# Optimization experiments

Hardware: AMD Instinct MI355X
Metric: run time of the kernel (lower is better)

Reference implementation:

```python
import jax, jax.numpy as jnp
import numpy as np

I_DIM, H_DIM, SEQ, OUT = 2048, 2048, 4096, 2048

def setup_inputs() -> dict:
    key = jax.random.key(0)
    ks = jax.random.split(key, 8)
    s_i = 1.0 / np.sqrt(H_DIM)
    return {
        "input_seq": jax.random.normal(ks[0], (1, SEQ, I_DIM), dtype=jnp.float32),
        "W_ih": jax.random.uniform(ks[1], (4 * H_DIM, I_DIM), minval=-s_i, maxval=s_i, dtype=jnp.float32),
        "W_hh": jax.random.uniform(ks[2], (4 * H_DIM, H_DIM), minval=-s_i, maxval=s_i, dtype=jnp.float32),
        "b_ih": jax.random.uniform(ks[3], (4 * H_DIM,), minval=-s_i, maxval=s_i, dtype=jnp.float32),
        "b_hh": jax.random.uniform(ks[4], (4 * H_DIM,), minval=-s_i, maxval=s_i, dtype=jnp.float32),
        "W_fc": jax.random.uniform(ks[5], (OUT, H_DIM), minval=-s_i, maxval=s_i, dtype=jnp.float32),
        "b_fc": jax.random.uniform(ks[6], (OUT,), minval=-s_i, maxval=s_i, dtype=jnp.float32),
    }

def _lstm_last_h(x, W_ih, W_hh, b_ih, b_hh):
    # x: [B, S, I]. PyTorch gate order: i, f, g, o along the 4H axis.
    B, S, _ = x.shape
    H = W_hh.shape[1]
    # Precompute input contribution for all timesteps: [B, S, 4H]
    xg = jnp.einsum('bsi,gi->bsg', x, W_ih) + b_ih + b_hh

    def step(carry, xg_t):
        h, c = carry  # [B, H] each
        g = xg_t + h @ W_hh.T  # [B, 4H]
        i_g = jax.nn.sigmoid(g[:, 0 * H:1 * H])
        f_g = jax.nn.sigmoid(g[:, 1 * H:2 * H])
        g_g = jnp.tanh(g[:, 2 * H:3 * H])
        o_g = jax.nn.sigmoid(g[:, 3 * H:4 * H])
        c = f_g * c + i_g * g_g
        h = o_g * jnp.tanh(c)
        return (h, c), None

    h0 = jnp.zeros((B, H), dtype=x.dtype)
    c0 = jnp.zeros((B, H), dtype=x.dtype)
    (h_last, _), _ = jax.lax.scan(step, (h0, c0), jnp.swapaxes(xg, 0, 1))
    return h_last  # [B, H]

def reference(input_seq, W_ih, W_hh, b_ih, b_hh, W_fc, b_fc):
    h_last = _lstm_last_h(input_seq, W_ih, W_hh, b_ih, b_hh)
    # Original does predictions.view(1, -1) then fc; valid only for batch=1.
    pred = h_last.reshape(1, -1) @ W_fc.T + b_fc  # [1, OUT]
    return pred
```

## Files before the change

### kernel.cpp

```cpp
#include <hip/hip_runtime.h>
#include <hip/hip_bf16.h>
#include <hip/hip_fp16.h>

#define SEQ   4096
#define IDIM  2048
#define HDIM  2048
#define G4    8192
#define NBLK  256
#define NREP  8

typedef __attribute__((ext_vector_type(8))) short short8;
typedef __attribute__((ext_vector_type(4))) float f32x4;

__device__ __forceinline__ float fast_sig(float x) {
    float e = __builtin_amdgcn_exp2f(-1.4426950408889634f * x);
    return __builtin_amdgcn_rcpf(1.0f + e);
}
__device__ __forceinline__ float fast_tanh(float x) {
    float e = __builtin_amdgcn_exp2f(2.8853900817779268f * x);
    return 1.0f - 2.0f * __builtin_amdgcn_rcpf(e + 1.0f);
}
__device__ __forceinline__ unsigned short f2h(float f) {
    __half h = __float2half_rn(f);
    union { __half h; unsigned short s; } c; c.h = h; return c.s;
}
__device__ __forceinline__ float h2f(unsigned short u) {
    union { unsigned short s; __half h; } c; c.s = u; return __half2float(c.h);
}

#define GM 128
#define GN 128
#define GK 32
#define APAD 40

__global__ __launch_bounds__(256, 2)
void xg_gemm(const float* __restrict__ x, const float* __restrict__ Wih,
             const float* __restrict__ bih, const float* __restrict__ bhh,
             __hip_bfloat16* __restrict__ xg)
{
    __shared__ __hip_bfloat16 As[GM][APAD];
    __shared__ __hip_bfloat16 Bs[GN][APAD];

    const int t  = threadIdx.x;
    const int g0 = blockIdx.x * GN;
    const int s0 = blockIdx.y * GM;
    const int w  = t >> 6, L = t & 63;
    const int quad = L >> 4, lane16 = L & 15;
    const int wm = w >> 1, wn = w & 1;

    f32x4 acc[4][4];
#pragma unroll
    for (int mt = 0; mt < 4; ++mt)
#pragma unroll
        for (int nt = 0; nt < 4; ++nt) acc[mt][nt] = (f32x4){0.f, 0.f, 0.f, 0.f};

    const int srow = t >> 1, shalf = t & 1;
    const float* xp = x   + (size_t)(s0 + srow) * IDIM + 16 * shalf;
    const float* wp = Wih + (size_t)(g0 + srow) * IDIM + 16 * shalf;

    for (int k0 = 0; k0 < IDIM; k0 += GK) {
        float4 a0 = *(const float4*)(xp + k0);
        float4 a1 = *(const float4*)(xp + k0 + 4);
        float4 a2 = *(const float4*)(xp + k0 + 8);
        float4 a3 = *(const float4*)(xp + k0 + 12);
        float4 b0 = *(const float4*)(wp + k0);
        float4 b1 = *(const float4*)(wp + k0 + 4);
        float4 b2 = *(const float4*)(wp + k0 + 8);
        float4 b3 = *(const float4*)(wp + k0 + 12);
        __syncthreads();
        {
            union { __hip_bfloat16 h[8]; uint4 u; } pk;
            pk.h[0]=__float2bfloat16(a0.x); pk.h[1]=__float2bfloat16(a0.y);
            pk.h[2]=__float2bfloat16(a0.z); pk.h[3]=__float2bfloat16(a0.w);
            pk.h[4]=__float2bfloat16(a1.x); pk.h[5]=__float2bfloat16(a1.y);
            pk.h[6]=__float2bfloat16(a1.z); pk.h[7]=__float2bfloat16(a1.w);
            *(uint4*)&As[srow][16 * shalf] = pk.u;
            pk.h[0]=__float2bfloat16(a2.x); pk.h[1]=__float2bfloat16(a2.y);
            pk.h[2]=__float2bfloat16(a2.z); pk.h[3]=__float2bfloat16(a2.w);
            pk.h[4]=__float2bfloat16(a3.x); pk.h[5]=__float2bfloat16(a3.y);
            pk.h[6]=__float2bfloat16(a3.z); pk.h[7]=__float2bfloat16(a3.w);
            *(uint4*)&As[srow][16 * shalf + 8] = pk.u;
            pk.h[0]=__float2bfloat16(b0.x); pk.h[1]=__float2bfloat16(b0.y);
            pk.h[2]=__float2bfloat16(b0.z); pk.h[3]=__float2bfloat16(b0.w);
            pk.h[4]=__float2bfloat16(b1.x); pk.h[5]=__float2bfloat16(b1.y);
            pk.h[6]=__float2bfloat16(b1.z); pk.h[7]=__float2bfloat16(b1.w);
            *(uint4*)&Bs[srow][16 * shalf] = pk.u;
            pk.h[0]=__float2bfloat16(b2.x); pk.h[1]=__float2bfloat16(b2.y);
            pk.h[2]=__float2bfloat16(b2.z); pk.h[3]=__float2bfloat16(b2.w);
            pk.h[4]=__float2bfloat16(b3.x); pk.h[5]=__float2bfloat16(b3.y);
            pk.h[6]=__float2bfloat16(b3.z); pk.h[7]=__float2bfloat16(b3.w);
            *(uint4*)&Bs[srow][16 * shalf + 8] = pk.u;
        }
        __syncthreads();

        short8 af[4], bf[4];
#pragma unroll
        for (int mt = 0; mt < 4; ++mt)
            af[mt] = *(const short8*)&As[wm * 64 + mt * 16 + lane16][quad * 8];
#pragma unroll
        for (int nt = 0; nt < 4; ++nt)
            bf[nt] = *(const short8*)&Bs[wn * 64 + nt * 16 + lane16][quad * 8];
#pragma unroll
        for (int mt = 0; mt < 4; ++mt)
#pragma unroll
            for (int nt = 0; nt < 4; ++nt)
                acc[mt][nt] = __builtin_amdgcn_mfma_f32_16x16x32_bf16(
                                  af[mt], bf[nt], acc[mt][nt], 0, 0, 0);
    }

#pragma unroll
    for (int nt = 0; nt < 4; ++nt) {
        const int g = g0 + wn * 64 + nt * 16 + lane16;
        const float bias = bih[g] + bhh[g];
#pragma unroll
        for (int mt = 0; mt < 4; ++mt) {
#pragma unroll
            for (int r = 0; r < 4; ++r) {
                const int so = s0 + wm * 64 + mt * 16 + quad * 4 + r;
                xg[(size_t)so * G4 + g] = __float2bfloat16(acc[mt][nt][r] + bias);
            }
        }
    }
}

__global__ __launch_bounds__(256, 1)
void lstm_rec(const float* __restrict__ Whh,
              const __hip_bfloat16* __restrict__ xg,
              float* __restrict__ hout,
              unsigned long long* __restrict__ msg)
{
    __shared__ float hsh[2][HDIM];
    __shared__ int   flag[4];

    const int t  = threadIdx.x;
    const int b  = blockIdx.x;
    const int w  = t >> 6;
    const int L  = t & 63;
    const int hi = L & 1;
    const int rb = b & (NREP - 1);

    float4 wv[8][8];
#pragma unroll
    for (int r = 0; r < 8; ++r) {
        const float* rp = Whh + (size_t)((r >> 1) * HDIM + 8 * b + 2 * w + (r & 1)) * HDIM + 4 * L;
#pragma unroll
        for (int i = 0; i < 4; ++i) {
            const int c = w ^ i;
#pragma unroll
            for (int u = 0; u < 2; ++u)
                wv[r][2 * i + u] = *(const float4*)(rp + 512 * c + 256 * u);
        }
    }

    if (t < 4) flag[t] = -1;
    float creg = 0.0f;
    float xq0, xq1, xq2, xq3;
    {
        const size_t xb = (size_t)(8 * b + 2 * w + hi);
        xq0 = __bfloat162float(xg[xb]);
        xq1 = __bfloat162float(xg[xb + HDIM]);
        xq2 = __bfloat162float(xg[xb + 2 * HDIM]);
        xq3 = __bfloat162float(xg[xb + 3 * HDIM]);
    }
    __syncthreads();

    for (int s = 0; s < SEQ; ++s) {
        const int pb = s & 1;

        float f0,f1,f2,f3,f4,f5,f6,f7;
        if (s == 0) {
            f0=f1=f2=f3=f4=f5=f6=f7 = 0.0f;
        } else {
            const unsigned long long* p0 = &msg[(size_t)((pb * NREP + rb) * 4 + 0) * NBLK + t];
            const unsigned long long* p1 = &msg[(size_t)((pb * NREP + rb) * 4 + 1) * NBLK + t];
            const unsigned long long* p2 = &msg[(size_t)((pb * NREP + rb) * 4 + 2) * NBLK + t];
            const unsigned long long* p3 = &msg[(size_t)((pb * NREP + rb) * 4 + 3) * NBLK + t];
            const unsigned tgt = (unsigned)s;
            unsigned long long v0, v1, v2, v3;
            do {
                v0 = __hip_atomic_load(p0, __ATOMIC_RELAXED, __HIP_MEMORY_SCOPE_AGENT);
                v1 = __hip_atomic_load(p1, __ATOMIC_RELAXED, __HIP_MEMORY_SCOPE_AGENT);
                v2 = __hip_atomic_load(p2, __ATOMIC_RELAXED, __HIP_MEMORY_SCOPE_AGENT);
                v3 = __hip_atomic_load(p3, __ATOMIC_RELAXED, __HIP_MEMORY_SCOPE_AGENT);
            } while (min(min((unsigned)(v0 & 0xFFFFu), (unsigned)(v1 & 0xFFFFu)),
                         min((unsigned)(v2 & 0xFFFFu), (unsigned)(v3 & 0xFFFFu))) < tgt);
            f0 = h2f((unsigned short)(v0 >> 16));
            f1 = h2f((unsigned short)(v0 >> 32));
            f2 = h2f((unsigned short)(v1 >> 16));
            f3 = h2f((unsigned short)(v1 >> 32));
            f4 = h2f((unsigned short)(v2 >> 16));
            f5 = h2f((unsigned short)(v2 >> 32));
            f6 = h2f((unsigned short)(v3 >> 16));
            f7 = h2f((unsigned short)(v3 >> 32));
        }
        float4 hv0 = { f0, f1, f2, f3 };
        float4 hv1 = { f4, f5, f6, f7 };
        *(float4*)&hsh[pb][8 * t]     = hv0;
        *(float4*)&hsh[pb][8 * t + 4] = hv1;
        if (L == 0)
            __hip_atomic_store(&flag[w], s, __ATOMIC_RELEASE, __HIP_MEMORY_SCOPE_WORKGROUP);

        float a0=0.f,a1=0.f,a2=0.f,a3=0.f,a4=0.f,a5=0.f,a6=0.f,a7=0.f;
#pragma unroll
        for (int i = 0; i < 4; ++i) {
            const int c = w ^ i;
            if (i != 0) {
                while (__hip_atomic_load(&flag[c], __ATOMIC_ACQUIRE,
                                         __HIP_MEMORY_SCOPE_WORKGROUP) < s) {}
            }
#pragma unroll
            for (int u = 0; u < 2; ++u) {
                const int q = 2 * i + u;
                float4 hv = *(const float4*)&hsh[pb][4 * L + 512 * c + 256 * u];
                a0 += wv[0][q].x*hv.x; a0 += wv[0][q].y*hv.y; a0 += wv[0][q].z*hv.z; a0 += wv[0][q].w*hv.w;
                a1 += wv[1][q].x*hv.x; a1 += wv[1][q].y*hv.y; a1 += wv[1][q].z*hv.z; a1 += wv[1][q].w*hv.w;
                a2 += wv[2][q].x*hv.x; a2 += wv[2][q].y*hv.y; a2 += wv[2][q].z*hv.z; a2 += wv[2][q].w*hv.w;
                a3 += wv[3][q].x*hv.x; a3 += wv[3][q].y*hv.y; a3 += wv[3][q].z*hv.z; a3 += wv[3][q].w*hv.w;
                a4 += wv[4][q].x*hv.x; a4 += wv[4][q].y*hv.y; a4 += wv[4][q].z*hv.z; a4 += wv[4][q].w*hv.w;
                a5 += wv[5][q].x*hv.x; a5 += wv[5][q].y*hv.y; a5 += wv[5][q].z*hv.z; a5 += wv[5][q].w*hv.w;
                a6 += wv[6][q].x*hv.x; a6 += wv[6][q].y*hv.y; a6 += wv[6][q].z*hv.z; a6 += wv[6][q].w*hv.w;
                a7 += wv[7][q].x*hv.x; a7 += wv[7][q].y*hv.y; a7 += wv[7][q].z*hv.z; a7 += wv[7][q].w*hv.w;
            }
        }

        float g0v = (hi ? a1 : a0) + __shfl_xor(hi ? a0 : a1, 1, 64);
        float g1v = (hi ? a3 : a2) + __shfl_xor(hi ? a2 : a3, 1, 64);
        float g2v = (hi ? a5 : a4) + __shfl_xor(hi ? a4 : a5, 1, 64);
        float g3v = (hi ? a7 : a6) + __shfl_xor(hi ? a6 : a7, 1, 64);
#pragma unroll
        for (int m = 2; m <= 32; m <<= 1) {
            g0v += __shfl_xor(g0v, m, 64);
            g1v += __shfl_xor(g1v, m, 64);
            g2v += __shfl_xor(g2v, m, 64);
            g3v += __shfl_xor(g3v, m, 64);
        }
        float pi = g0v + xq0;
        float pf = g1v + xq1;
        float pg = g2v + xq2;
        float po = g3v + xq3;

        float cn = fast_sig(pf) * creg + fast_sig(pi) * fast_tanh(pg);
        creg = cn;
        float h = fast_sig(po) * fast_tanh(cn);
        if (s == SEQ - 1 && L < 2) hout[8 * b + 2 * w + L] = h;

        if (s + 1 < SEQ) {
            const int p = (s + 1) & 1;
            float hp = __shfl_xor(h, 1, 64);
            float h0 = hi ? hp : h;
            float h1 = hi ? h : hp;
            if (L < NREP) {
                unsigned long long u = (unsigned long long)(unsigned short)(s + 1)
                    | ((unsigned long long)f2h(h0) << 16)
                    | ((unsigned long long)f2h(h1) << 32);
                __hip_atomic_store(
                        &msg[(size_t)((p * NREP + L) * 4 + w) * NBLK + b], u,
                        __ATOMIC_RELAXED, __HIP_MEMORY_SCOPE_AGENT);
            }
            const size_t xb = (size_t)(s + 1) * G4 + 8 * b + 2 * w + hi;
            xq0 = __bfloat162float(xg[xb]);
            xq1 = __bfloat162float(xg[xb + HDIM]);
            xq2 = __bfloat162float(xg[xb + 2 * HDIM]);
            xq3 = __bfloat162float(xg[xb + 3 * HDIM]);
        }
    }
}

__global__ __launch_bounds__(64)
void fc_kernel(const float* __restrict__ h, const float* __restrict__ Wfc,
               const float* __restrict__ bfc, float* __restrict__ out)
{
    const int o = blockIdx.x;
    const int L = threadIdx.x;
    const float* wr = Wfc + (size_t)o * HDIM;
    float s = 0.0f;
#pragma unroll
    for (int jj = 0; jj < 8; ++jj) {
        float4 wvv = *(const float4*)(wr + 4 * (L + 64 * jj));
        float4 hv  = *(const float4*)(h  + 4 * (L + 64 * jj));
        s += wvv.x * hv.x + wvv.y * hv.y + wvv.z * hv.z + wvv.w * hv.w;
    }
#pragma unroll
    for (int mask = 1; mask <= 32; mask <<= 1) s += __shfl_xor(s, mask, 64);
    if (L == 0) out[o] = s + bfc[o];
}

extern "C" void kernel_launch(void* const* d_in, const int* in_sizes, int n_in,
                              void* d_out, int out_size, void* d_ws, size_t ws_size,
                              hipStream_t stream)
{
    (void)in_sizes; (void)n_in; (void)out_size; (void)ws_size;
    const float* x   = (const float*)d_in[0];
    const float* Wih = (const float*)d_in[1];
    const float* Whh = (const float*)d_in[2];
    const float* bih = (const float*)d_in[3];
    const float* bhh = (const float*)d_in[4];
    const float* Wfc = (const float*)d_in[5];
    const float* bfc = (const float*)d_in[6];
    float* out = (float*)d_out;

    __hip_bfloat16* xg       = (__hip_bfloat16*)d_ws;
    float* hout              = (float*)((char*)d_ws + (size_t)SEQ * G4 * sizeof(__hip_bfloat16));
    unsigned long long* msg  = (unsigned long long*)(hout + HDIM);

    (void)hipMemsetAsync(msg, 0, (size_t)2 * NREP * 4 * NBLK * sizeof(unsigned long long), stream);

    dim3 g1(G4 / GN, SEQ / GM);
    hipLaunchKernelGGL(xg_gemm, g1, dim3(256), 0, stream, x, Wih, bih, bhh, xg);

    float* hout_arg = hout;
    unsigned long long* msg_arg = msg;
    void* args[] = { (void*)&Whh, (void*)&xg, (void*)&hout_arg, (void*)&msg_arg };
    hipError_t ce = hipLaunchCooperativeKernel((const void*)lstm_rec, dim3(NBLK), dim3(256),
                                               args, 0, stream);
    if (ce != hipSuccess) {
        hipLaunchKernelGGL(lstm_rec, dim3(NBLK), dim3(256), 0, stream, Whh, xg, hout, msg);
    }

    hipLaunchKernelGGL(fc_kernel, dim3(2048), dim3(64), 0, stream, hout, Wfc, bfc, out);
}
```

Baseline: 13.01 ms.

## Halve recurrent grid to 128 blocks of 512 threads with 8 waves each

The persistent LSTM recurrence now runs 128 workgroups of 8 waves instead of 256 workgroups of 4 waves. Each block owns 16 hidden units, and each wave still holds 8 W_hh rows in registers. The message layout is re-indexed for 8 units per block, and each thread polls 2 slots instead of 4. This halves the number of blocks in the cross-block exchange and the polling traffic per thread, at the cost of more intra-block flag waits and only one block per CU across fewer CUs.

```diff
diff --git a/kernel.cpp b/kernel.cpp
--- a/kernel.cpp
+++ b/kernel.cpp
@@ -6,7 +6,9 @@
 #define IDIM  2048
 #define HDIM  2048
 #define G4    8192
-#define NBLK  256
+#define NBLK  128
+#define TPB   512
+#define NUNIT 8
 #define NREP  8
 
 typedef __attribute__((ext_vector_type(8))) short short8;
@@ -123,18 +125,18 @@
     }
 }
 
-__global__ __launch_bounds__(256, 1)
+__global__ __launch_bounds__(512, 1)
 void lstm_rec(const float* __restrict__ Whh,
               const __hip_bfloat16* __restrict__ xg,
               float* __restrict__ hout,
               unsigned long long* __restrict__ msg)
 {
     __shared__ float hsh[2][HDIM];
-    __shared__ int   flag[4];
+    __shared__ int   flag[8];
 
     const int t  = threadIdx.x;
     const int b  = blockIdx.x;
-    const int w  = t >> 6;
+    const int W  = t >> 6;
     const int L  = t & 63;
     const int hi = L & 1;
     const int rb = b & (NREP - 1);
@@ -142,21 +144,19 @@
     float4 wv[8][8];
 #pragma unroll
     for (int r = 0; r < 8; ++r) {
-        const float* rp = Whh + (size_t)((r >> 1) * HDIM + 8 * b + 2 * w + (r & 1)) * HDIM + 4 * L;
-#pragma unroll
-        for (int i = 0; i < 4; ++i) {
-            const int c = w ^ i;
-#pragma unroll
-            for (int u = 0; u < 2; ++u)
-                wv[r][2 * i + u] = *(const float4*)(rp + 512 * c + 256 * u);
-        }
-    }
-
-    if (t < 4) flag[t] = -1;
+        const float* rp = Whh + (size_t)((r >> 1) * HDIM + 16 * b + 2 * W + (r & 1)) * HDIM + 4 * L;
+#pragma unroll
+        for (int i = 0; i < 8; ++i) {
+            const int c = W ^ i;
+            wv[r][i] = *(const float4*)(rp + 256 * c);
+        }
+    }
+
+    if (t < 8) flag[t] = -1;
     float creg = 0.0f;
     float xq0, xq1, xq2, xq3;
     {
-        const size_t xb = (size_t)(8 * b + 2 * w + hi);
+        const size_t xb = (size_t)(16 * b + 2 * W + hi);
         xq0 = __bfloat162float(xg[xb]);
         xq1 = __bfloat162float(xg[xb + HDIM]);
         xq2 = __bfloat162float(xg[xb + 2 * HDIM]);
@@ -167,60 +167,47 @@
     for (int s = 0; s < SEQ; ++s) {
         const int pb = s & 1;
 
-        float f0,f1,f2,f3,f4,f5,f6,f7;
+        float f0,f1,f2,f3;
         if (s == 0) {
-            f0=f1=f2=f3=f4=f5=f6=f7 = 0.0f;
+            f0=f1=f2=f3 = 0.0f;
         } else {
-            const unsigned long long* p0 = &msg[(size_t)((pb * NREP + rb) * 4 + 0) * NBLK + t];
-            const unsigned long long* p1 = &msg[(size_t)((pb * NREP + rb) * 4 + 1) * NBLK + t];
-            const unsigned long long* p2 = &msg[(size_t)((pb * NREP + rb) * 4 + 2) * NBLK + t];
-            const unsigned long long* p3 = &msg[(size_t)((pb * NREP + rb) * 4 + 3) * NBLK + t];
+            const int p  = t >> 2;
+            const int u0 = 2 * (t & 3);
+            const unsigned long long* q0 = &msg[(size_t)((pb * NREP + rb) * NUNIT + u0) * NBLK + p];
+            const unsigned long long* q1 = q0 + NBLK;
             const unsigned tgt = (unsigned)s;
-            unsigned long long v0, v1, v2, v3;
+            unsigned long long v0, v1;
             do {
-                v0 = __hip_atomic_load(p0, __ATOMIC_RELAXED, __HIP_MEMORY_SCOPE_AGENT);
-                v1 = __hip_atomic_load(p1, __ATOMIC_RELAXED, __HIP_MEMORY_SCOPE_AGENT);
-                v2 = __hip_atomic_load(p2, __ATOMIC_RELAXED, __HIP_MEMORY_SCOPE_AGENT);
-                v3 = __hip_atomic_load(p3, __ATOMIC_RELAXED, __HIP_MEMORY_SCOPE_AGENT);
-            } while (min(min((unsigned)(v0 & 0xFFFFu), (unsigned)(v1 & 0xFFFFu)),
-                         min((unsigned)(v2 & 0xFFFFu), (unsigned)(v3 & 0xFFFFu))) < tgt);
+                v0 = __hip_atomic_load(q0, __ATOMIC_RELAXED, __HIP_MEMORY_SCOPE_AGENT);
+                v1 = __hip_atomic_load(q1, __ATOMIC_RELAXED, __HIP_MEMORY_SCOPE_AGENT);
+            } while (min((unsigned)(v0 & 0xFFFFu), (unsigned)(v1 & 0xFFFFu)) < tgt);
             f0 = h2f((unsigned short)(v0 >> 16));
             f1 = h2f((unsigned short)(v0 >> 32));
             f2 = h2f((unsigned short)(v1 >> 16));
             f3 = h2f((unsigned short)(v1 >> 32));
-            f4 = h2f((unsigned short)(v2 >> 16));
-            f5 = h2f((unsigned short)(v2 >> 32));
-            f6 = h2f((unsigned short)(v3 >> 16));
-            f7 = h2f((unsigned short)(v3 >> 32));
         }
         float4 hv0 = { f0, f1, f2, f3 };
-        float4 hv1 = { f4, f5, f6, f7 };
-        *(float4*)&hsh[pb][8 * t]     = hv0;
-        *(float4*)&hsh[pb][8 * t + 4] = hv1;
+        *(float4*)&hsh[pb][4 * t] = hv0;
         if (L == 0)
-            __hip_atomic_store(&flag[w], s, __ATOMIC_RELEASE, __HIP_MEMORY_SCOPE_WORKGROUP);
+            __hip_atomic_store(&flag[W], s, __ATOMIC_RELEASE, __HIP_MEMORY_SCOPE_WORKGROUP);
 
         float a0=0.f,a1=0.f,a2=0.f,a3=0.f,a4=0.f,a5=0.f,a6=0.f,a7=0.f;
 #pragma unroll
-        for (int i = 0; i < 4; ++i) {
-            const int c = w ^ i;
+        for (int i = 0; i < 8; ++i) {
+            const int c = W ^ i;
             if (i != 0) {
                 while (__hip_atomic_load(&flag[c], __ATOMIC_ACQUIRE,
                                          __HIP_MEMORY_SCOPE_WORKGROUP) < s) {}
             }
-#pragma unroll
-            for (int u = 0; u < 2; ++u) {
-                const int q = 2 * i + u;
-                float4 hv = *(const float4*)&hsh[pb][4 * L + 512 * c + 256 * u];
-                a0 += wv[0][q].x*hv.x; a0 += wv[0][q].y*hv.y; a0 += wv[0][q].z*hv.z; a0 += wv[0][q].w*hv.w;
-                a1 += wv[1][q].x*hv.x; a1 += wv[1][q].y*hv.y; a1 += wv[1][q].z*hv.z; a1 += wv[1][q].w*hv.w;
-                a2 += wv[2][q].x*hv.x; a2 += wv[2][q].y*hv.y; a2 += wv[2][q].z*hv.z; a2 += wv[2][q].w*hv.w;
-                a3 += wv[3][q].x*hv.x; a3 += wv[3][q].y*hv.y; a3 += wv[3][q].z*hv.z; a3 += wv[3][q].w*hv.w;
-                a4 += wv[4][q].x*hv.x; a4 += wv[4][q].y*hv.y; a4 += wv[4][q].z*hv.z; a4 += wv[4][q].w*hv.w;
-                a5 += wv[5][q].x*hv.x; a5 += wv[5][q].y*hv.y; a5 += wv[5][q].z*hv.z; a5 += wv[5][q].w*hv.w;
-                a6 += wv[6][q].x*hv.x; a6 += wv[6][q].y*hv.y; a6 += wv[6][q].z*hv.z; a6 += wv[6][q].w*hv.w;
-                a7 += wv[7][q].x*hv.x; a7 += wv[7][q].y*hv.y; a7 += wv[7][q].z*hv.z; a7 += wv[7][q].w*hv.w;
-            }
+            float4 hv = *(const float4*)&hsh[pb][4 * L + 256 * c];
+            a0 += wv[0][i].x*hv.x; a0 += wv[0][i].y*hv.y; a0 += wv[0][i].z*hv.z; a0 += wv[0][i].w*hv.w;
+            a1 += wv[1][i].x*hv.x; a1 += wv[1][i].y*hv.y; a1 += wv[1][i].z*hv.z; a1 += wv[1][i].w*hv.w;
+            a2 += wv[2][i].x*hv.x; a2 += wv[2][i].y*hv.y; a2 += wv[2][i].z*hv.z; a2 += wv[2][i].w*hv.w;
+            a3 += wv[3][i].x*hv.x; a3 += wv[3][i].y*hv.y; a3 += wv[3][i].z*hv.z; a3 += wv[3][i].w*hv.w;
+            a4 += wv[4][i].x*hv.x; a4 += wv[4][i].y*hv.y; a4 += wv[4][i].z*hv.z; a4 += wv[4][i].w*hv.w;
+            a5 += wv[5][i].x*hv.x; a5 += wv[5][i].y*hv.y; a5 += wv[5][i].z*hv.z; a5 += wv[5][i].w*hv.w;
+            a6 += wv[6][i].x*hv.x; a6 += wv[6][i].y*hv.y; a6 += wv[6][i].z*hv.z; a6 += wv[6][i].w*hv.w;
+            a7 += wv[7][i].x*hv.x; a7 += wv[7][i].y*hv.y; a7 += wv[7][i].z*hv.z; a7 += wv[7][i].w*hv.w;
         }
 
         float g0v = (hi ? a1 : a0) + __shfl_xor(hi ? a0 : a1, 1, 64);
@@ -242,10 +229,10 @@
         float cn = fast_sig(pf) * creg + fast_sig(pi) * fast_tanh(pg);
         creg = cn;
         float h = fast_sig(po) * fast_tanh(cn);
-        if (s == SEQ - 1 && L < 2) hout[8 * b + 2 * w + L] = h;
+        if (s == SEQ - 1 && L < 2) hout[16 * b + 2 * W + L] = h;
 
         if (s + 1 < SEQ) {
-            const int p = (s + 1) & 1;
+            const int p2 = (s + 1) & 1;
             float hp = __shfl_xor(h, 1, 64);
             float h0 = hi ? hp : h;
             float h1 = hi ? h : hp;
@@ -254,10 +241,10 @@
                     | ((unsigned long long)f2h(h0) << 16)
                     | ((unsigned long long)f2h(h1) << 32);
                 __hip_atomic_store(
-                        &msg[(size_t)((p * NREP + L) * 4 + w) * NBLK + b], u,
+                        &msg[(size_t)((p2 * NREP + L) * NUNIT + W) * NBLK + b], u,
                         __ATOMIC_RELAXED, __HIP_MEMORY_SCOPE_AGENT);
             }
-            const size_t xb = (size_t)(s + 1) * G4 + 8 * b + 2 * w + hi;
+            const size_t xb = (size_t)(s + 1) * G4 + 16 * b + 2 * W + hi;
             xq0 = __bfloat162float(xg[xb]);
             xq1 = __bfloat162float(xg[xb + HDIM]);
             xq2 = __bfloat162float(xg[xb + 2 * HDIM]);
@@ -303,7 +290,7 @@
     float* hout              = (float*)((char*)d_ws + (size_t)SEQ * G4 * sizeof(__hip_bfloat16));
     unsigned long long* msg  = (unsigned long long*)(hout + HDIM);
 
-    (void)hipMemsetAsync(msg, 0, (size_t)2 * NREP * 4 * NBLK * sizeof(unsigned long long), stream);
+    (void)hipMemsetAsync(msg, 0, (size_t)2 * NREP * NUNIT * NBLK * sizeof(unsigned long long), stream);
 
     dim3 g1(G4 / GN, SEQ / GM);
     hipLaunchKernelGGL(xg_gemm, g1, dim3(256), 0, stream, x, Wih, bih, bhh, xg);
@@ -311,10 +298,10 @@
     float* hout_arg = hout;
     unsigned long long* msg_arg = msg;
     void* args[] = { (void*)&Whh, (void*)&xg, (void*)&hout_arg, (void*)&msg_arg };
-    hipError_t ce = hipLaunchCooperativeKernel((const void*)lstm_rec, dim3(NBLK), dim3(256),
+    hipError_t ce = hipLaunchCooperativeKernel((const void*)lstm_rec, dim3(NBLK), dim3(TPB),
                                                args, 0, stream);
     if (ce != hipSuccess) {
-        hipLaunchKernelGGL(lstm_rec, dim3(NBLK), dim3(256), 0, stream, Whh, xg, hout, msg);
+        hipLaunchKernelGGL(lstm_rec, dim3(NBLK), dim3(TPB), 0, stream, Whh, xg, hout, msg);
     }
 
     hipLaunchKernelGGL(fc_kernel, dim3(2048), dim3(64), 0, stream, hout, Wfc, bfc, out);
```

New measurement: 32.14 ms. +147.0%, slower.
